# Performance work log

Hardware: AMD Instinct MI355X
Metric: run time of the kernel (lower is better)

Reference implementation:

```python
import jax, jax.numpy as jnp
import numpy as np
from jax import lax

EPS = 1e-12  # F.normalize default eps


def _l2_normalize(v, axis=-1):
    n = jnp.linalg.norm(v, axis=axis, keepdims=True)
    return v / jnp.maximum(n, EPS)


def setup_inputs() -> dict:
    key = jax.random.key(0)
    k1, k2, k3 = jax.random.split(key, 3)
    x = jax.random.normal(k1, (4, 768, 4096), dtype=jnp.float32)
    conv_w = jax.random.normal(k2, (128, 768, 3), dtype=jnp.float32) * 0.02
    codebook = jax.random.normal(k3, (8192, 128), dtype=jnp.float32)
    return {"x": x, "conv_w": conv_w, "codebook": codebook}


def reference(x, conv_w, codebook):
    # in_proj: Conv1d(input_dim -> codebook_dim, k=3, stride=2, pad=1, no bias)
    x_e = lax.conv_general_dilated(
        x, conv_w,
        window_strides=(2,), padding=[(1, 1)],
        dimension_numbers=("NCH", "OIH", "NCH"),
    )  # [b, d, t]
    b, d, t = x_e.shape
    enc = _l2_normalize(x_e.transpose(0, 2, 1).reshape(b * t, d))  # [(b t), d]
    cb = _l2_normalize(codebook)                                    # [K, d]
    # dist = ||e||^2 - 2 e.c + ||c||^2
    dist = (
        jnp.sum(enc * enc, axis=1, keepdims=True)
        - 2.0 * enc @ cb.T
        + jnp.sum(cb * cb, axis=1)[None, :]
    )  # [(b t), K]
    indices = jnp.argmax(-dist, axis=1).reshape(b, t)
    return indices
```

## Files before the change

kernel.cpp:

```cpp
#include <hip/hip_runtime.h>

#define EPS 1e-12f

#define BATCH 4
#define CIN   768
#define LIN   4096
#define DCODE 128
#define TOUT  2048
#define NROWS (BATCH*TOUT)
#define KCB   8192
#define KCONV 2304

#define OFF_CN2  0u
#define OFF_BS   32768u
#define OFF_BI   163840u
#define OFF_EH   294912u
#define OFF_EL   2392064u
#define OFF_CH   4489216u
#define OFF_CL   6586368u
#define OFF_WHT  8683520u
#define OFF_WLT  9273344u
#define OFF_PART 9863168u
#define OFF_XTH  18251776u
#define OFF_XTL  43417600u

typedef _Float16 half_t;
typedef __attribute__((ext_vector_type(8))) _Float16 half8;
typedef __attribute__((ext_vector_type(2))) _Float16 half2v;
typedef __attribute__((ext_vector_type(4))) float f32x4;

__global__ __launch_bounds__(256) void k_wt2(const float* __restrict__ w,
                                             half_t* __restrict__ wht,
                                             half_t* __restrict__ wlt) {
    int k = blockIdx.x * 256 + threadIdx.x;
    int n = blockIdx.y;
    if (k >= KCONV) return;
    int j = (k >= 1536) ? 2 : (k >= 768) ? 1 : 0;
    int c = k - j * 768;
    float v = w[(size_t)n * KCONV + c * 3 + j];
    half_t h = (half_t)v;
    wht[(size_t)n * KCONV + k] = h;
    wlt[(size_t)n * KCONV + k] = (half_t)(v - (float)h);
}

__global__ __launch_bounds__(256) void k_xt(const float* __restrict__ x,
                                            half_t* __restrict__ xth,
                                            half_t* __restrict__ xtl) {
    __shared__ float tile[32][33];
    const int s0 = blockIdx.x * 32;
    const int c0 = blockIdx.y * 32;
    const int b  = blockIdx.z;
    const int sl = threadIdx.x & 31;
    const int cl = threadIdx.x >> 5;
    const float* xg = x + ((size_t)b * CIN + c0) * LIN + s0;
    #pragma unroll
    for (int p = 0; p < 4; ++p) {
        int c = cl + p * 8;
        tile[c][sl] = xg[(size_t)c * LIN + sl];
    }
    __syncthreads();
    const int wcc = (threadIdx.x & 15) * 2;
    const int wss = threadIdx.x >> 4;
    #pragma unroll
    for (int p = 0; p < 2; ++p) {
        int s = wss + p * 16;
        float v0 = tile[wcc][s], v1 = tile[wcc + 1][s];
        half_t h0 = (half_t)v0, h1 = (half_t)v1;
        half_t l0 = (half_t)(v0 - (float)h0), l1 = (half_t)(v1 - (float)h1);
        size_t o = ((size_t)b * LIN + s0 + s) * CIN + c0 + wcc;
        *(half2v*)(xth + o) = half2v{h0, h1};
        *(half2v*)(xtl + o) = half2v{l0, l1};
    }
}

__global__ __launch_bounds__(256) void k_cbnorm(const float* __restrict__ cb,
                                                half_t* __restrict__ ch,
                                                half_t* __restrict__ cl,
                                                float* __restrict__ cn2) {
    int wid  = threadIdx.x >> 6;
    int lane = threadIdx.x & 63;
    int k = blockIdx.x * 4 + wid;
    const float2* src = (const float2*)cb + (size_t)k * 64;
    float2 v = src[lane];
    float ss = v.x * v.x + v.y * v.y;
    #pragma unroll
    for (int m = 1; m < 64; m <<= 1) ss += __shfl_xor(ss, m);
    float inv = 1.0f / fmaxf(sqrtf(ss), EPS);
    float nx = v.x * inv, ny = v.y * inv;
    half_t hx = (half_t)nx, hy = (half_t)ny;
    half_t lx = (half_t)(nx - (float)hx), ly = (half_t)(ny - (float)hy);
    ((half2v*)ch)[(size_t)k * 64 + lane] = half2v{hx, hy};
    ((half2v*)cl)[(size_t)k * 64 + lane] = half2v{lx, ly};
    if (lane == 0) cn2[k] = ss * inv * inv;
}

__global__ __launch_bounds__(256, 1) void k_conv_mfma(
        const half_t* __restrict__ xth, const half_t* __restrict__ xtl,
        const half_t* __restrict__ wht, const half_t* __restrict__ wlt,
        float* __restrict__ part) {
    extern __shared__ char smem[];
    const int tid  = threadIdx.x;
    const int lane = tid & 63;
    const int w    = tid >> 6;
    const int wr   = w >> 1;
    const int wc   = w & 1;
    const int lr   = lane & 15;
    const int lg   = lane >> 4;
    const int r0   = blockIdx.x * 64;
    const int ks   = blockIdx.y;
    const int b    = r0 >> 11;
    const int t00  = r0 & 2047;
    const int kbase = ks * 1152;

    const half_t* msrc = (w >> 1) ? wlt : wht;
    auto stage = [&](int t, int buf) {
        int k0 = kbase + t * 128;
        #pragma unroll
        for (int i = 0; i < 16; ++i) {
            int col_l = (w & 1) * 64 + i * 4 + lg;
            int ksrc  = (lr * 16) ^ ((col_l & 7) << 4);
            const char* g = (const char*)msrc + (size_t)col_l * 4608
                          + (size_t)k0 * 2 + ksrc;
            char* l = smem + buf * 65536 + w * 16384 + i * 1024;
            __builtin_amdgcn_global_load_lds(
                (const __attribute__((address_space(1))) void*)(uintptr_t)g,
                (__attribute__((address_space(3))) void*)(uintptr_t)l, 16, 0, 0);
        }
    };

    f32x4 acc[2][4];
    #pragma unroll
    for (int g = 0; g < 2; ++g)
        #pragma unroll
        for (int cg = 0; cg < 4; ++cg) acc[g][cg] = f32x4{0.f, 0.f, 0.f, 0.f};

    stage(0, 0);
    __syncthreads();

    int buf = 0;
    for (int t = 0; t < 9; ++t) {
        int k0 = kbase + t * 128;
        int j  = (k0 >= 1536) ? 2 : (k0 >= 768) ? 1 : 0;
        int c0 = k0 - j * 768;
        half8 ah[2][4], al[2][4];
        #pragma unroll
        for (int g = 0; g < 2; ++g) {
            int trow = t00 + wr * 32 + g * 16 + lr;
            int s = 2 * trow - 1 + j;
            bool valid = (unsigned)s < (unsigned)LIN;
            size_t o = ((size_t)b * LIN + (valid ? s : 0)) * CIN + c0 + lg * 8;
            const half8* ph = (const half8*)(xth + o);
            const half8* pl = (const half8*)(xtl + o);
            #pragma unroll
            for (int kc = 0; kc < 4; ++kc) {
                half8 vh = {}, vl = {};
                if (valid) { vh = ph[kc * 4]; vl = pl[kc * 4]; }
                ah[g][kc] = vh; al[g][kc] = vl;
            }
        }
        if (t < 8) stage(t + 1, buf ^ 1);
        const char* bhp = smem + buf * 65536;
        const char* blp = bhp + 32768;
        #pragma unroll
        for (int kc = 0; kc < 4; ++kc) {
            half8 bhf[4], blf[4];
            #pragma unroll
            for (int cg = 0; cg < 4; ++cg) {
                int col   = wc * 64 + cg * 16 + lr;
                int kswz  = (col & 7) << 4;
                int cbyte = col * 256;
                int kb    = (kc * 64 + lg * 16) ^ kswz;
                bhf[cg] = *(const half8*)(bhp + cbyte + kb);
                blf[cg] = *(const half8*)(blp + cbyte + kb);
            }
            #pragma unroll
            for (int cg = 0; cg < 4; ++cg)
                #pragma unroll
                for (int g = 0; g < 2; ++g)
                    acc[g][cg] = __builtin_amdgcn_mfma_f32_16x16x32_f16(ah[g][kc], bhf[cg], acc[g][cg], 0, 0, 0);
            #pragma unroll
            for (int cg = 0; cg < 4; ++cg)
                #pragma unroll
                for (int g = 0; g < 2; ++g)
                    acc[g][cg] = __builtin_amdgcn_mfma_f32_16x16x32_f16(al[g][kc], bhf[cg], acc[g][cg], 0, 0, 0);
            #pragma unroll
            for (int cg = 0; cg < 4; ++cg)
                #pragma unroll
                for (int g = 0; g < 2; ++g)
                    acc[g][cg] = __builtin_amdgcn_mfma_f32_16x16x32_f16(ah[g][kc], blf[cg], acc[g][cg], 0, 0, 0);
        }
        __syncthreads();
        buf ^= 1;
    }

    float* pb = part + (size_t)ks * NROWS * DCODE;
    #pragma unroll
    for (int g = 0; g < 2; ++g)
        #pragma unroll
        for (int cg = 0; cg < 4; ++cg) {
            int col = wc * 64 + cg * 16 + lr;
            #pragma unroll
            for (int rr = 0; rr < 4; ++rr) {
                int row = r0 + wr * 32 + g * 16 + lg * 4 + rr;
                pb[(size_t)row * DCODE + col] = acc[g][cg][rr];
            }
        }
}

__global__ __launch_bounds__(256) void k_encnorm(const float* __restrict__ part,
                                                 half_t* __restrict__ eh,
                                                 half_t* __restrict__ el) {
    int wid  = threadIdx.x >> 6;
    int lane = threadIdx.x & 63;
    int r = blockIdx.x * 4 + wid;
    const float2* p0 = (const float2*)part + (size_t)r * 64;
    const float2* p1 = (const float2*)(part + (size_t)NROWS * DCODE) + (size_t)r * 64;
    float2 a = p0[lane];
    float2 c = p1[lane];
    a.x += c.x; a.y += c.y;
    float ss = a.x * a.x + a.y * a.y;
    #pragma unroll
    for (int m = 1; m < 64; m <<= 1) ss += __shfl_xor(ss, m);
    float inv = 1.0f / fmaxf(sqrtf(ss), EPS);
    float nx = a.x * inv, ny = a.y * inv;
    half_t hx = (half_t)nx, hy = (half_t)ny;
    half_t lx = (half_t)(nx - (float)hx), ly = (half_t)(ny - (float)hy);
    ((half2v*)eh)[(size_t)r * 64 + lane] = half2v{hx, hy};
    ((half2v*)el)[(size_t)r * 64 + lane] = half2v{lx, ly};
}

__global__ __launch_bounds__(256, 1) void k_dist(const half_t* __restrict__ eh,
                                                 const half_t* __restrict__ el,
                                                 const half_t* __restrict__ ch,
                                                 const half_t* __restrict__ cl,
                                                 const float* __restrict__ cn2,
                                                 float* __restrict__ best_s,
                                                 int* __restrict__ best_i) {
    extern __shared__ char smem[];
    const int tid  = threadIdx.x;
    const int lane = tid & 63;
    const int w    = tid >> 6;
    const int lr   = lane & 15;
    const int lg   = lane >> 4;
    const int r0   = blockIdx.x * 64;
    const int kqbase = blockIdx.y * 4096;

    half8 ah[4][4], al[4][4];
    #pragma unroll
    for (int g = 0; g < 4; ++g) {
        int row = r0 + g * 16 + lr;
        const half8* ph = (const half8*)(eh + (size_t)row * 128 + lg * 8);
        const half8* pl = (const half8*)(el + (size_t)row * 128 + lg * 8);
        #pragma unroll
        for (int kc = 0; kc < 4; ++kc) { ah[g][kc] = ph[kc * 4]; al[g][kc] = pl[kc * 4]; }
    }

    const half_t* msrc = (w >> 1) ? cl : ch;
    auto stage = [&](int t, int buf) {
        #pragma unroll
        for (int i = 0; i < 16; ++i) {
            int col_l = (w & 1) * 64 + i * 4 + lg;
            int ksrc  = (lr * 16) ^ ((col_l & 7) << 4);
            const char* g = (const char*)msrc
                          + ((size_t)(kqbase + t * 128 + col_l)) * 256 + ksrc;
            char* l = smem + buf * 65536 + w * 16384 + i * 1024;
            __builtin_amdgcn_global_load_lds(
                (const __attribute__((address_space(1))) void*)(uintptr_t)g,
                (__attribute__((address_space(3))) void*)(uintptr_t)l, 16, 0, 0);
        }
    };

    float bs[4][4]; int bi[4][4];
    #pragma unroll
    for (int g = 0; g < 4; ++g)
        #pragma unroll
        for (int rr = 0; rr < 4; ++rr) { bs[g][rr] = -3.4e38f; bi[g][rr] = 0; }

    stage(0, 0);
    __syncthreads();

    int buf = 0;
    for (int t = 0; t < 32; ++t) {
        if (t < 31) stage(t + 1, buf ^ 1);
        float cnv[2];
        #pragma unroll
        for (int cg = 0; cg < 2; ++cg)
            cnv[cg] = cn2[kqbase + t * 128 + w * 32 + cg * 16 + lr];
        const char* bhp = smem + buf * 65536;
        const char* blp = bhp + 32768;
        f32x4 acc[4][2];
        #pragma unroll
        for (int g = 0; g < 4; ++g)
            #pragma unroll
            for (int cg = 0; cg < 2; ++cg) acc[g][cg] = f32x4{0.f, 0.f, 0.f, 0.f};
        #pragma unroll
        for (int kc = 0; kc < 4; ++kc) {
            half8 bhf[2], blf[2];
            #pragma unroll
            for (int cg = 0; cg < 2; ++cg) {
                int col   = w * 32 + cg * 16 + lr;
                int kswz  = (col & 7) << 4;
                int cbyte = col * 256;
                int kb    = (kc * 64 + lg * 16) ^ kswz;
                bhf[cg] = *(const half8*)(bhp + cbyte + kb);
                blf[cg] = *(const half8*)(blp + cbyte + kb);
            }
            #pragma unroll
            for (int cg = 0; cg < 2; ++cg)
                #pragma unroll
                for (int g = 0; g < 4; ++g)
                    acc[g][cg] = __builtin_amdgcn_mfma_f32_16x16x32_f16(ah[g][kc], bhf[cg], acc[g][cg], 0, 0, 0);
            #pragma unroll
            for (int cg = 0; cg < 2; ++cg)
                #pragma unroll
                for (int g = 0; g < 4; ++g)
                    acc[g][cg] = __builtin_amdgcn_mfma_f32_16x16x32_f16(al[g][kc], bhf[cg], acc[g][cg], 0, 0, 0);
            #pragma unroll
            for (int cg = 0; cg < 2; ++cg)
                #pragma unroll
                for (int g = 0; g < 4; ++g)
                    acc[g][cg] = __builtin_amdgcn_mfma_f32_16x16x32_f16(ah[g][kc], blf[cg], acc[g][cg], 0, 0, 0);
        }
        #pragma unroll
        for (int g = 0; g < 4; ++g)
            #pragma unroll
            for (int cg = 0; cg < 2; ++cg) {
                int n = kqbase + t * 128 + w * 32 + cg * 16 + lr;
                #pragma unroll
                for (int rr = 0; rr < 4; ++rr) {
                    float sc = 2.0f * acc[g][cg][rr] - cnv[cg];
                    if (sc > bs[g][rr]) { bs[g][rr] = sc; bi[g][rr] = n; }
                }
            }
        __syncthreads();
        buf ^= 1;
    }

    float* redS = (float*)smem;
    int*   redI = (int*)(smem + 1024);
    #pragma unroll
    for (int g = 0; g < 4; ++g)
        #pragma unroll
        for (int rr = 0; rr < 4; ++rr) {
            float s = bs[g][rr]; int i = bi[g][rr];
            #pragma unroll
            for (int m = 1; m < 16; m <<= 1) {
                float os = __shfl_xor(s, m);
                int   oi = __shfl_xor(i, m);
                if (os > s || (os == s && oi < i)) { s = os; i = oi; }
            }
            if (lr == 0) {
                int row = g * 16 + lg * 4 + rr;
                redS[w * 64 + row] = s;
                redI[w * 64 + row] = i;
            }
        }
    __syncthreads();
    if (tid < 64) {
        float s = redS[tid]; int i = redI[tid];
        #pragma unroll
        for (int w2 = 1; w2 < 4; ++w2) {
            float s2 = redS[w2 * 64 + tid];
            int   i2 = redI[w2 * 64 + tid];
            if (s2 > s || (s2 == s && i2 < i)) { s = s2; i = i2; }
        }
        best_s[(size_t)blockIdx.y * NROWS + r0 + tid] = s;
        best_i[(size_t)blockIdx.y * NROWS + r0 + tid] = i;
    }
}

__global__ __launch_bounds__(256) void k_merge(const float* __restrict__ bs,
                                               const int* __restrict__ bi,
                                               int* __restrict__ out) {
    int r = blockIdx.x * 256 + threadIdx.x;
    if (r >= NROWS) return;
    float s = bs[r]; int i = bi[r];
    #pragma unroll
    for (int q = 1; q < 2; ++q) {
        float s2 = bs[(size_t)q * NROWS + r];
        int   i2 = bi[(size_t)q * NROWS + r];
        if (s2 > s || (s2 == s && i2 < i)) { s = s2; i = i2; }
    }
    out[r] = i;
}

extern "C" void kernel_launch(void* const* d_in, const int* in_sizes, int n_in,
                              void* d_out, int out_size, void* d_ws, size_t ws_size,
                              hipStream_t stream) {
    const float* x  = (const float*)d_in[0];
    const float* w  = (const float*)d_in[1];
    const float* cb = (const float*)d_in[2];
    char* ws = (char*)d_ws;
    float*  cn2  = (float*)(ws + OFF_CN2);
    float*  bs   = (float*)(ws + OFF_BS);
    int*    bi   = (int*)(ws + OFF_BI);
    half_t* eh   = (half_t*)(ws + OFF_EH);
    half_t* el   = (half_t*)(ws + OFF_EL);
    half_t* chh  = (half_t*)(ws + OFF_CH);
    half_t* cll  = (half_t*)(ws + OFF_CL);
    half_t* wht  = (half_t*)(ws + OFF_WHT);
    half_t* wlt  = (half_t*)(ws + OFF_WLT);
    float*  part = (float*)(ws + OFF_PART);
    half_t* xth  = (half_t*)(ws + OFF_XTH);
    half_t* xtl  = (half_t*)(ws + OFF_XTL);
    int*    out  = (int*)d_out;

    hipFuncSetAttribute((const void*)k_dist,
                        hipFuncAttributeMaxDynamicSharedMemorySize, 131072);
    hipFuncSetAttribute((const void*)k_conv_mfma,
                        hipFuncAttributeMaxDynamicSharedMemorySize, 131072);

    k_wt2     <<<dim3(9, 128), 256, 0, stream>>>(w, wht, wlt);
    k_cbnorm  <<<2048, 256, 0, stream>>>(cb, chh, cll, cn2);
    k_xt      <<<dim3(128, 24, 4), 256, 0, stream>>>(x, xth, xtl);
    k_conv_mfma<<<dim3(128, 2), 256, 131072, stream>>>(xth, xtl, wht, wlt, part);
    k_encnorm <<<2048, 256, 0, stream>>>(part, eh, el);
    k_dist    <<<dim3(128, 2), 256, 131072, stream>>>(eh, el, chh, cll, cn2, bs, bi);
    k_merge   <<<32, 256, 0, stream>>>(bs, bi, out);
}
```

Before: 204.2 us.

## Double waves per block in conv and distance MFMA kernels

Both MFMA kernels (conv and distance) go from 256 to 512 threads per block. Each wave now covers half as many output columns, and the global-to-LDS staging is split across eight waves. The aim is more waves per CU to hide memory and MFMA latency while keeping the same grid and shared-memory tiles. The cost is more redundant A-fragment loads per block, since each wave reloads the rows, plus a larger cross-wave reduction in the distance kernel. The launch_bounds(512,2) hint cannot actually give two blocks per CU when each block uses 128KB of LDS.

Measured after the change: 212.4 us. +4.0%, slower.

```diff
diff --git a/kernel.cpp b/kernel.cpp
--- a/kernel.cpp
+++ b/kernel.cpp
@@ -94,7 +94,7 @@
     if (lane == 0) cn2[k] = ss * inv * inv;
 }
 
-__global__ __launch_bounds__(256, 1) void k_conv_mfma(
+__global__ __launch_bounds__(512, 2) void k_conv_mfma(
         const half_t* __restrict__ xth, const half_t* __restrict__ xtl,
         const half_t* __restrict__ wht, const half_t* __restrict__ wlt,
         float* __restrict__ part) {
@@ -102,8 +102,8 @@
     const int tid  = threadIdx.x;
     const int lane = tid & 63;
     const int w    = tid >> 6;
-    const int wr   = w >> 1;
-    const int wc   = w & 1;
+    const int rg   = w >> 2;
+    const int cgw  = w & 3;
     const int lr   = lane & 15;
     const int lg   = lane >> 4;
     const int r0   = blockIdx.x * 64;
@@ -112,27 +112,29 @@
     const int t00  = r0 & 2047;
     const int kbase = ks * 1152;
 
-    const half_t* msrc = (w >> 1) ? wlt : wht;
+    const half_t* msrc = (w >= 4) ? wlt : wht;
+    const int wmod = w & 3;
     auto stage = [&](int t, int buf) {
         int k0 = kbase + t * 128;
         #pragma unroll
-        for (int i = 0; i < 16; ++i) {
-            int col_l = (w & 1) * 64 + i * 4 + lg;
+        for (int i = 0; i < 8; ++i) {
+            int col_l = wmod * 32 + i * 4 + lg;
             int ksrc  = (lr * 16) ^ ((col_l & 7) << 4);
             const char* g = (const char*)msrc + (size_t)col_l * 4608
                           + (size_t)k0 * 2 + ksrc;
-            char* l = smem + buf * 65536 + w * 16384 + i * 1024;
+            char* l = smem + buf * 65536 + (w >> 2) * 32768 + wmod * 8192
+                    + i * 1024;
             __builtin_amdgcn_global_load_lds(
                 (const __attribute__((address_space(1))) void*)(uintptr_t)g,
                 (__attribute__((address_space(3))) void*)(uintptr_t)l, 16, 0, 0);
         }
     };
 
-    f32x4 acc[2][4];
+    f32x4 acc[2][2];
     #pragma unroll
     for (int g = 0; g < 2; ++g)
         #pragma unroll
-        for (int cg = 0; cg < 4; ++cg) acc[g][cg] = f32x4{0.f, 0.f, 0.f, 0.f};
+        for (int cg = 0; cg < 2; ++cg) acc[g][cg] = f32x4{0.f, 0.f, 0.f, 0.f};
 
     stage(0, 0);
     __syncthreads();
@@ -145,7 +147,7 @@
         half8 ah[2][4], al[2][4];
         #pragma unroll
         for (int g = 0; g < 2; ++g) {
-            int trow = t00 + wr * 32 + g * 16 + lr;
+            int trow = t00 + rg * 32 + g * 16 + lr;
             int s = 2 * trow - 1 + j;
             bool valid = (unsigned)s < (unsigned)LIN;
             size_t o = ((size_t)b * LIN + (valid ? s : 0)) * CIN + c0 + lg * 8;
@@ -163,10 +165,10 @@
         const char* blp = bhp + 32768;
         #pragma unroll
         for (int kc = 0; kc < 4; ++kc) {
-            half8 bhf[4], blf[4];
-            #pragma unroll
-            for (int cg = 0; cg < 4; ++cg) {
-                int col   = wc * 64 + cg * 16 + lr;
+            half8 bhf[2], blf[2];
+            #pragma unroll
+            for (int cg = 0; cg < 2; ++cg) {
+                int col   = cgw * 32 + cg * 16 + lr;
                 int kswz  = (col & 7) << 4;
                 int cbyte = col * 256;
                 int kb    = (kc * 64 + lg * 16) ^ kswz;
@@ -174,17 +176,17 @@
                 blf[cg] = *(const half8*)(blp + cbyte + kb);
             }
             #pragma unroll
-            for (int cg = 0; cg < 4; ++cg)
+            for (int cg = 0; cg < 2; ++cg)
                 #pragma unroll
                 for (int g = 0; g < 2; ++g)
                     acc[g][cg] = __builtin_amdgcn_mfma_f32_16x16x32_f16(ah[g][kc], bhf[cg], acc[g][cg], 0, 0, 0);
             #pragma unroll
-            for (int cg = 0; cg < 4; ++cg)
+            for (int cg = 0; cg < 2; ++cg)
                 #pragma unroll
                 for (int g = 0; g < 2; ++g)
                     acc[g][cg] = __builtin_amdgcn_mfma_f32_16x16x32_f16(al[g][kc], bhf[cg], acc[g][cg], 0, 0, 0);
             #pragma unroll
-            for (int cg = 0; cg < 4; ++cg)
+            for (int cg = 0; cg < 2; ++cg)
                 #pragma unroll
                 for (int g = 0; g < 2; ++g)
                     acc[g][cg] = __builtin_amdgcn_mfma_f32_16x16x32_f16(ah[g][kc], blf[cg], acc[g][cg], 0, 0, 0);
@@ -197,11 +199,11 @@
     #pragma unroll
     for (int g = 0; g < 2; ++g)
         #pragma unroll
-        for (int cg = 0; cg < 4; ++cg) {
-            int col = wc * 64 + cg * 16 + lr;
+        for (int cg = 0; cg < 2; ++cg) {
+            int col = cgw * 32 + cg * 16 + lr;
             #pragma unroll
             for (int rr = 0; rr < 4; ++rr) {
-                int row = r0 + wr * 32 + g * 16 + lg * 4 + rr;
+                int row = r0 + rg * 32 + g * 16 + lg * 4 + rr;
                 pb[(size_t)row * DCODE + col] = acc[g][cg][rr];
             }
         }
@@ -229,7 +231,7 @@
     ((half2v*)el)[(size_t)r * 64 + lane] = half2v{lx, ly};
 }
 
-__global__ __launch_bounds__(256, 1) void k_dist(const half_t* __restrict__ eh,
+__global__ __launch_bounds__(512, 2) void k_dist(const half_t* __restrict__ eh,
                                                  const half_t* __restrict__ el,
                                                  const half_t* __restrict__ ch,
                                                  const half_t* __restrict__ cl,
@@ -255,15 +257,17 @@
         for (int kc = 0; kc < 4; ++kc) { ah[g][kc] = ph[kc * 4]; al[g][kc] = pl[kc * 4]; }
     }
 
-    const half_t* msrc = (w >> 1) ? cl : ch;
+    const half_t* msrc = (w >= 4) ? cl : ch;
+    const int wmod = w & 3;
     auto stage = [&](int t, int buf) {
         #pragma unroll
-        for (int i = 0; i < 16; ++i) {
-            int col_l = (w & 1) * 64 + i * 4 + lg;
+        for (int i = 0; i < 8; ++i) {
+            int col_l = wmod * 32 + i * 4 + lg;
             int ksrc  = (lr * 16) ^ ((col_l & 7) << 4);
             const char* g = (const char*)msrc
                           + ((size_t)(kqbase + t * 128 + col_l)) * 256 + ksrc;
-            char* l = smem + buf * 65536 + w * 16384 + i * 1024;
+            char* l = smem + buf * 65536 + (w >> 2) * 32768 + wmod * 8192
+                    + i * 1024;
             __builtin_amdgcn_global_load_lds(
                 (const __attribute__((address_space(1))) void*)(uintptr_t)g,
                 (__attribute__((address_space(3))) void*)(uintptr_t)l, 16, 0, 0);
@@ -282,62 +286,44 @@
     int buf = 0;
     for (int t = 0; t < 32; ++t) {
         if (t < 31) stage(t + 1, buf ^ 1);
-        float cnv[2];
-        #pragma unroll
-        for (int cg = 0; cg < 2; ++cg)
-            cnv[cg] = cn2[kqbase + t * 128 + w * 32 + cg * 16 + lr];
+        int n = kqbase + t * 128 + w * 16 + lr;
+        float cnv = cn2[n];
         const char* bhp = smem + buf * 65536;
         const char* blp = bhp + 32768;
-        f32x4 acc[4][2];
+        f32x4 acc[4];
+        #pragma unroll
+        for (int g = 0; g < 4; ++g) acc[g] = f32x4{0.f, 0.f, 0.f, 0.f};
+        const int col   = w * 16 + lr;
+        const int kswz  = (col & 7) << 4;
+        const int cbyte = col * 256;
+        #pragma unroll
+        for (int kc = 0; kc < 4; ++kc) {
+            int kb = (kc * 64 + lg * 16) ^ kswz;
+            half8 bhf = *(const half8*)(bhp + cbyte + kb);
+            half8 blf = *(const half8*)(blp + cbyte + kb);
+            #pragma unroll
+            for (int g = 0; g < 4; ++g)
+                acc[g] = __builtin_amdgcn_mfma_f32_16x16x32_f16(ah[g][kc], bhf, acc[g], 0, 0, 0);
+            #pragma unroll
+            for (int g = 0; g < 4; ++g)
+                acc[g] = __builtin_amdgcn_mfma_f32_16x16x32_f16(al[g][kc], bhf, acc[g], 0, 0, 0);
+            #pragma unroll
+            for (int g = 0; g < 4; ++g)
+                acc[g] = __builtin_amdgcn_mfma_f32_16x16x32_f16(ah[g][kc], blf, acc[g], 0, 0, 0);
+        }
         #pragma unroll
         for (int g = 0; g < 4; ++g)
             #pragma unroll
-            for (int cg = 0; cg < 2; ++cg) acc[g][cg] = f32x4{0.f, 0.f, 0.f, 0.f};
-        #pragma unroll
-        for (int kc = 0; kc < 4; ++kc) {
-            half8 bhf[2], blf[2];
-            #pragma unroll
-            for (int cg = 0; cg < 2; ++cg) {
-                int col   = w * 32 + cg * 16 + lr;
-                int kswz  = (col & 7) << 4;
-                int cbyte = col * 256;
-                int kb    = (kc * 64 + lg * 16) ^ kswz;
-                bhf[cg] = *(const half8*)(bhp + cbyte + kb);
-                blf[cg] = *(const half8*)(blp + cbyte + kb);
-            }
-            #pragma unroll
-            for (int cg = 0; cg < 2; ++cg)
-                #pragma unroll
-                for (int g = 0; g < 4; ++g)
-                    acc[g][cg] = __builtin_amdgcn_mfma_f32_16x16x32_f16(ah[g][kc], bhf[cg], acc[g][cg], 0, 0, 0);
-            #pragma unroll
-            for (int cg = 0; cg < 2; ++cg)
-                #pragma unroll
-                for (int g = 0; g < 4; ++g)
-                    acc[g][cg] = __builtin_amdgcn_mfma_f32_16x16x32_f16(al[g][kc], bhf[cg], acc[g][cg], 0, 0, 0);
-            #pragma unroll
-            for (int cg = 0; cg < 2; ++cg)
-                #pragma unroll
-                for (int g = 0; g < 4; ++g)
-                    acc[g][cg] = __builtin_amdgcn_mfma_f32_16x16x32_f16(ah[g][kc], blf[cg], acc[g][cg], 0, 0, 0);
-        }
-        #pragma unroll
-        for (int g = 0; g < 4; ++g)
-            #pragma unroll
-            for (int cg = 0; cg < 2; ++cg) {
-                int n = kqbase + t * 128 + w * 32 + cg * 16 + lr;
-                #pragma unroll
-                for (int rr = 0; rr < 4; ++rr) {
-                    float sc = 2.0f * acc[g][cg][rr] - cnv[cg];
-                    if (sc > bs[g][rr]) { bs[g][rr] = sc; bi[g][rr] = n; }
-                }
+            for (int rr = 0; rr < 4; ++rr) {
+                float sc = 2.0f * acc[g][rr] - cnv;
+                if (sc > bs[g][rr]) { bs[g][rr] = sc; bi[g][rr] = n; }
             }
         __syncthreads();
         buf ^= 1;
     }
 
     float* redS = (float*)smem;
-    int*   redI = (int*)(smem + 1024);
+    int*   redI = (int*)(smem + 2048);
     #pragma unroll
     for (int g = 0; g < 4; ++g)
         #pragma unroll
@@ -359,7 +345,7 @@
     if (tid < 64) {
         float s = redS[tid]; int i = redI[tid];
         #pragma unroll
-        for (int w2 = 1; w2 < 4; ++w2) {
+        for (int w2 = 1; w2 < 8; ++w2) {
             float s2 = redS[w2 * 64 + tid];
             int   i2 = redI[w2 * 64 + tid];
             if (s2 > s || (s2 == s && i2 < i)) { s = s2; i = i2; }
@@ -413,8 +399,8 @@
     k_wt2     <<<dim3(9, 128), 256, 0, stream>>>(w, wht, wlt);
     k_cbnorm  <<<2048, 256, 0, stream>>>(cb, chh, cll, cn2);
     k_xt      <<<dim3(128, 24, 4), 256, 0, stream>>>(x, xth, xtl);
-    k_conv_mfma<<<dim3(128, 2), 256, 131072, stream>>>(xth, xtl, wht, wlt, part);
+    k_conv_mfma<<<dim3(128, 2), 512, 131072, stream>>>(xth, xtl, wht, wlt, part);
     k_encnorm <<<2048, 256, 0, stream>>>(part, eh, el);
-    k_dist    <<<dim3(128, 2), 256, 131072, stream>>>(eh, el, chh, cll, cn2, bs, bi);
+    k_dist    <<<dim3(128, 2), 512, 131072, stream>>>(eh, el, chh, cll, cn2, bs, bi);
     k_merge   <<<32, 256, 0, stream>>>(bs, bi, out);
 }
```
